# Kernel tuning notes

Hardware: AMD Instinct MI355X
Metric: run time of the kernel (lower is better)

Reference implementation:

```python
import jax, jax.numpy as jnp
import numpy as np

TEMPERATURE = 0.1
NEG_INF = -1e30  # finite sentinel so masked logsumexp has zero (not NaN) gradient


def setup_inputs() -> dict:
    key = jax.random.key(0)
    k1, k2, k3 = jax.random.split(key, 3)
    N, D = 8192, 512          # flattened (batch * TRs) trials, feature dim
    NUM_CLASSES = 3           # vigilance states
    return {
        "objs_feats": jax.random.normal(k1, (N, D), dtype=jnp.float32),
        "objs_labels": jax.random.randint(k2, (N,), 0, NUM_CLASSES, dtype=jnp.int32),
        "bad_tr": jax.random.randint(k3, (N,), 0, 2, dtype=jnp.int32),
    }


def reference(objs_feats, objs_labels, bad_tr):
    # Faithful vectorization of SetCriterion.contrastive_loss_batch_without_break.
    N = objs_feats.shape[0]
    f = objs_feats / jnp.linalg.norm(objs_feats, axis=-1, keepdims=True)
    S = (f @ f.T) / TEMPERATURE                      # [N, N] cosine-sim logits

    valid = bad_tr == 0                              # [N]
    same = objs_labels[:, None] == objs_labels[None, :]
    eye = jnp.eye(N, dtype=bool)
    neg_mask = valid[None, :] & (~same)              # [N, N] negatives per anchor
    pos_mask = valid[None, :] & same & (~eye)        # [N, N] positives per anchor

    has_neg = neg_mask.any(axis=1)
    has_pos = pos_mask.any(axis=1)
    processed = valid & has_neg                      # anchors the loop doesn't `continue` past

    # logsumexp over negatives of each anchor row
    neg_lse = jax.nn.logsumexp(jnp.where(neg_mask, S, NEG_INF), axis=1)  # [N]

    # anchors WITH positives: CE over rows [S[i,p], S[i, negs...]] with target 0,
    # averaged over positives p -> mean_p( logaddexp(S[i,p], neg_lse_i) - S[i,p] )
    ce_per_pos = jnp.logaddexp(S, neg_lse[:, None]) - S                  # [N, N]
    pos_cnt = pos_mask.sum(axis=1)
    loss_with_pos = jnp.where(pos_mask, ce_per_pos, 0.0).sum(axis=1) / jnp.maximum(pos_cnt, 1)

    # anchors WITHOUT positives: pos logit is the constant 1/temperature
    inv_t = jnp.float32(1.0 / TEMPERATURE)
    loss_no_pos = jnp.logaddexp(inv_t, neg_lse) - inv_t

    per_anchor = jnp.where(has_pos, loss_with_pos, loss_no_pos)
    total = jnp.where(processed, per_anchor, 0.0).sum()
    # valid_obj_cnt starts at 1; no-pos anchors net to 0 (−1 then +1)
    count = 1 + (processed & has_pos).sum()
    return total / count.astype(total.dtype)
```

## Files before the change

### kernel.cpp

```cpp
#include <hip/hip_runtime.h>

typedef __bf16 bf16x8 __attribute__((ext_vector_type(8)));
typedef __bf16 bf16x4 __attribute__((ext_vector_type(4)));
typedef float f32x4 __attribute__((ext_vector_type(4)));

#define SLOTW 260

#define GLOAD_LDS16(g, l)                                                      \
  __builtin_amdgcn_global_load_lds(                                            \
      (const __attribute__((address_space(1))) void*)(g),                      \
      (__attribute__((address_space(3))) void*)(l), 16, 0, 0)

__global__ __launch_bounds__(1024) void k_scan(
    const int* __restrict__ labels, const int* __restrict__ bad,
    unsigned char* __restrict__ code, int* __restrict__ dst,
    int* __restrict__ hdr, __bf16* __restrict__ fng,
    unsigned char* __restrict__ gcode, float* __restrict__ out, int Nv,
    int Dv) {
  const int t = threadIdx.x;
  const int lane = t & 63, wv = t >> 6;
  const int per = Nv >> 10;
  const int base = t * per;
  unsigned char lc[8];
  int cnt[3] = {0, 0, 0};
  for (int k = 0; k < per; ++k) {
    const int r = base + k;
    const unsigned char c =
        (bad[r] == 0) ? (unsigned char)labels[r] : (unsigned char)255;
    lc[k] = c;
    code[r] = c;
    if (c <= 2) cnt[c]++;
  }
  int inc0 = cnt[0], inc1 = cnt[1], inc2 = cnt[2];
#pragma unroll
  for (int off = 1; off < 64; off <<= 1) {
    const int a = __shfl_up(inc0, off);
    const int b = __shfl_up(inc1, off);
    const int c = __shfl_up(inc2, off);
    if (lane >= off) {
      inc0 += a;
      inc1 += b;
      inc2 += c;
    }
  }
  __shared__ int wt[16][3], wo[17][3];
  if (lane == 63) {
    wt[wv][0] = inc0;
    wt[wv][1] = inc1;
    wt[wv][2] = inc2;
  }
  __syncthreads();
  if (t == 0) {
    int s0 = 0, s1 = 0, s2 = 0;
    for (int w = 0; w < 16; ++w) {
      wo[w][0] = s0;
      wo[w][1] = s1;
      wo[w][2] = s2;
      s0 += wt[w][0];
      s1 += wt[w][1];
      s2 += wt[w][2];
    }
    wo[16][0] = s0;
    wo[16][1] = s1;
    wo[16][2] = s2;
  }
  __syncthreads();
  const int C0 = wo[16][0], C1 = wo[16][1], C2 = wo[16][2];
  int run[3];
  run[0] = wo[wv][0] + inc0 - cnt[0];
  run[1] = C0 + wo[wv][1] + inc1 - cnt[1];
  run[2] = C0 + C1 + wo[wv][2] + inc2 - cnt[2];
  for (int k = 0; k < per; ++k) {
    const int c = lc[k];
    dst[base + k] = (c <= 2) ? run[c]++ : -1;
  }
  const int M = C0 + C1 + C2;
  const int Mpad = (M + 127) & ~127;
  if (t == 0) {
    const int NTv = Mpad >> 7;
    hdr[0] = M;
    hdr[1] = Mpad;
    hdr[2] = NTv;
    hdr[3] = NTv * (NTv + 1) / 2;
    hdr[4] = C0;
    hdr[5] = C1;
    hdr[6] = C2;
    int count = 1;
    if (C0 >= 2 && M > C0) count += C0;
    if (C1 >= 2 && M > C1) count += C1;
    if (C2 >= 2 && M > C2) count += C2;
    hdr[7] = count;
    out[0] = 0.f;
  }
  for (int i = M + t; i < Mpad; i += 1024) gcode[i] = 255;
  const int nv4 = (Mpad - M) * (Dv >> 3);
  float4* fp = (float4*)(fng + (size_t)M * Dv);
  const float4 z = {0.f, 0.f, 0.f, 0.f};
  for (int i = t; i < nv4; i += 1024) fp[i] = z;
}

__global__ __launch_bounds__(128) void k_norm(const float* __restrict__ X,
                                              const unsigned char* __restrict__
                                                  code,
                                              const int* __restrict__ dst,
                                              __bf16* __restrict__ fng,
                                              unsigned char* __restrict__ gcode,
                                              int Dv) {
  const int row = blockIdx.x;
  const unsigned char c = code[row];
  if (c > 2) return;
  const int g = dst[row];
  const int t = threadIdx.x;
  const float4* xr = (const float4*)(X + (size_t)row * Dv);
  const int nv4 = Dv >> 2;
  __shared__ float sred[2];
  if (nv4 == 128) {
    const float4 v = xr[t];
    float ss = v.x * v.x + v.y * v.y + v.z * v.z + v.w * v.w;
#pragma unroll
    for (int off = 32; off; off >>= 1) ss += __shfl_down(ss, off);
    if ((t & 63) == 0) sred[t >> 6] = ss;
    __syncthreads();
    const float inv = 1.0f / sqrtf(sred[0] + sred[1]);
    bf16x4 o;
    o[0] = (__bf16)(v.x * inv);
    o[1] = (__bf16)(v.y * inv);
    o[2] = (__bf16)(v.z * inv);
    o[3] = (__bf16)(v.w * inv);
    *(bf16x4*)(fng + (size_t)g * Dv + t * 4) = o;
    if (t == 0) gcode[g] = c;
    return;
  }
  float ss = 0.f;
  for (int idx = t; idx < nv4; idx += 128) {
    float4 v = xr[idx];
    ss += v.x * v.x + v.y * v.y + v.z * v.z + v.w * v.w;
  }
#pragma unroll
  for (int off = 32; off; off >>= 1) ss += __shfl_down(ss, off);
  if ((t & 63) == 0) sred[t >> 6] = ss;
  __syncthreads();
  const float inv = 1.0f / sqrtf(sred[0] + sred[1]);
  const int nv8 = Dv >> 3;
  for (int idx = t; idx < nv8; idx += 128) {
    const float4 v0 = xr[idx * 2];
    const float4 v1 = xr[idx * 2 + 1];
    bf16x8 o;
    o[0] = (__bf16)(v0.x * inv);
    o[1] = (__bf16)(v0.y * inv);
    o[2] = (__bf16)(v0.z * inv);
    o[3] = (__bf16)(v0.w * inv);
    o[4] = (__bf16)(v1.x * inv);
    o[5] = (__bf16)(v1.y * inv);
    o[6] = (__bf16)(v1.z * inv);
    o[7] = (__bf16)(v1.w * inv);
    *(bf16x8*)(fng + (size_t)g * Dv + idx * 8) = o;
  }
  if (t == 0) gcode[g] = c;
}

__device__ __forceinline__ void tri_decode(int blk, int NT, int& bi, int& bj) {
  int b = 0, rem = blk, span = NT;
  while (rem >= span) {
    rem -= span;
    b++;
    span--;
  }
  bi = b;
  bj = b + rem;
}

__device__ __forceinline__ bool tile_overlap(const unsigned char* gcode,
                                             size_t sA, int lastA,
                                             size_t rowB) {
  const int la0 = gcode[sA], la1 = gcode[sA + lastA];
  const int lb0 = gcode[rowB], lb1 = gcode[rowB + 127];
  const int hiA = la1 > 2 ? 2 : la1;
  const int hiB = lb1 > 2 ? 2 : lb1;
  const int lo = la0 > lb0 ? la0 : lb0;
  const int hi = hiA < hiB ? hiA : hiB;
  return (la0 <= 2) && (lb0 <= 2) && (lo <= hi);
}

__global__ __launch_bounds__(512, 6) void k_p1(
    const __bf16* __restrict__ fng, const unsigned char* __restrict__ gcode,
    const int* __restrict__ hdr, float* __restrict__ P,
    _Float16* __restrict__ Sc, int Dv) {
  const int NTv = hdr[2];
  const int ntri = hdr[3];
  int bid = blockIdx.x;
  if (bid >= ntri) return;
  {
    const int q = ntri >> 3, r = ntri & 7, x = bid & 7, o = bid >> 3;
    bid = (x < r ? x * (q + 1) : r * (q + 1) + (x - r) * q) + o;
  }
  int bi, bj;
  tri_decode(bid, NTv, bi, bj);
  const size_t sA = (size_t)bi * 128;
  const size_t rowB = (size_t)bj * 128;
  __shared__ __align__(16) __bf16 As[2][128 * 32];
  __shared__ __align__(16) __bf16 Bs[2][128 * 32];

  const int t = threadIdx.x;
  const int lane = t & 63;
  const int wave = t >> 6;
  const int quad = lane >> 4;
  const int l16 = lane & 15;
  const int wr = (wave >> 1) * 32;
  const int wc = (wave & 1) * 64;
  const int r4 = t >> 2, q4 = t & 3;

  f32x4 acc[2][4] = {};
  auto stage = [&](int k0, int b) {
    GLOAD_LDS16(fng + (sA + r4) * Dv + k0 + q4 * 8,
                &As[b][(size_t)wave * 64 * 8]);
    GLOAD_LDS16(fng + (rowB + r4) * Dv + k0 + q4 * 8,
                &Bs[b][(size_t)wave * 64 * 8]);
  };
  stage(0, 0);
  int buf = 0;
  for (int k0 = 0; k0 < Dv; k0 += 32) {
    __syncthreads();
    if (k0 + 32 < Dv) stage(k0 + 32, buf ^ 1);
    bf16x8 af[2], bfv[4];
#pragma unroll
    for (int mi = 0; mi < 2; ++mi)
      af[mi] = *(const bf16x8*)&As[buf][(wr + mi * 16 + l16) * 32 + quad * 8];
#pragma unroll
    for (int ni = 0; ni < 4; ++ni)
      bfv[ni] = *(const bf16x8*)&Bs[buf][(wc + ni * 16 + l16) * 32 + quad * 8];
#pragma unroll
    for (int mi = 0; mi < 2; ++mi)
#pragma unroll
      for (int ni = 0; ni < 4; ++ni)
        acc[mi][ni] = __builtin_amdgcn_mfma_f32_16x16x32_bf16(
            af[mi], bfv[ni], acc[mi][ni], 0, 0, 0);
    buf ^= 1;
  }

  unsigned char ca[8], cb[4];
#pragma unroll
  for (int mi = 0; mi < 2; ++mi)
#pragma unroll
    for (int r = 0; r < 4; ++r)
      ca[mi * 4 + r] = gcode[sA + wr + mi * 16 + quad * 4 + r];
#pragma unroll
  for (int ni = 0; ni < 4; ++ni) cb[ni] = gcode[rowB + wc + ni * 16 + l16];
  const bool ov = tile_overlap(gcode, sA, 127, rowB);
  _Float16* St = Sc + (size_t)bid * 16384;

  float rowsum[8] = {};
  float colsum[4] = {};
#pragma unroll
  for (int mi = 0; mi < 2; ++mi)
#pragma unroll
    for (int ni = 0; ni < 4; ++ni)
#pragma unroll
      for (int r = 0; r < 4; ++r) {
        const float s = acc[mi][ni][r] * 10.0f;
        const float ex = __expf(s);
        const int a = ca[mi * 4 + r], b = cb[ni];
        const bool diff = a != b;
        rowsum[mi * 4 + r] += (b <= 2 && diff) ? ex : 0.f;
        colsum[ni] += (a <= 2 && diff) ? ex : 0.f;
        if (ov)
          St[(wr + mi * 16 + quad * 4 + r) * 128 + wc + ni * 16 + l16] =
              (_Float16)s;
      }
#pragma unroll
  for (int off = 1; off < 16; off <<= 1)
#pragma unroll
    for (int k = 0; k < 8; ++k) rowsum[k] += __shfl_xor(rowsum[k], off);
  if (l16 == 0)
#pragma unroll
    for (int k = 0; k < 8; ++k) {
      const size_t base =
          (sA + wr + (k >> 2) * 16 + quad * 4 + (k & 3)) * SLOTW + bj * 4;
      P[base + (wave & 1)] = rowsum[k];
      P[base + 2 + (wave & 1)] = 0.f;
    }
  if (bi != bj) {
#pragma unroll
    for (int off = 16; off < 64; off <<= 1)
#pragma unroll
      for (int ni = 0; ni < 4; ++ni) colsum[ni] += __shfl_xor(colsum[ni], off);
    if (quad == 0)
#pragma unroll
      for (int ni = 0; ni < 4; ++ni)
        P[(rowB + wc + ni * 16 + l16) * SLOTW + bi * 4 + (wave >> 1)] =
            colsum[ni];
  }
}

__global__ __launch_bounds__(256) void k_red(const float* __restrict__ P,
                                             float* __restrict__ out,
                                             const int* __restrict__ hdr,
                                             int Nv) {
  const int g = blockIdx.x * 256 + threadIdx.x;
  if (g >= Nv || g >= hdr[1]) return;
  const int ns = hdr[2] * 4;
  float s = 0.f;
  const float4* p = (const float4*)(P + (size_t)g * SLOTW);
  for (int k = 0; k < (ns >> 2); ++k) {
    const float4 v = p[k];
    s += v.x + v.y + v.z + v.w;
  }
  out[g] = s;
}

__global__ __launch_bounds__(256) void k_p2(
    const unsigned char* __restrict__ gcode, const int* __restrict__ hdr,
    const float* __restrict__ E, float* __restrict__ P2,
    const _Float16* __restrict__ Sc) {
  const int NTv = hdr[2];
  if ((int)blockIdx.x >= hdr[3]) return;
  int bi, bj;
  tri_decode(blockIdx.x, NTv, bi, bj);
  const int h = blockIdx.y;
  const size_t sA = (size_t)bi * 128 + h * 64;
  const size_t rowB = (size_t)bj * 128;
  const int t = threadIdx.x;
  const bool diag = (bi == bj);

  if (!tile_overlap(gcode, sA, 63, rowB)) {
    if (t < 64) {
      const size_t base = (sA + t) * SLOTW + bj * 4;
      P2[base] = 0.f;
      P2[base + 1] = 0.f;
      P2[base + 2] = 0.f;
      P2[base + 3] = 0.f;
    } else if (t < 192 && !diag) {
      const size_t base = (rowB + t - 64) * SLOTW + bi * 4 + h * 2;
      P2[base] = 0.f;
      P2[base + 1] = 0.f;
    }
    return;
  }

  const _Float16* St = Sc + ((size_t)blockIdx.x * 2 + h) * 8192;
  const int l8 = t & 15;
  unsigned char cb[8];
  float eB[8];
  {
    const uint2 cv = *(const uint2*)(gcode + rowB + l8 * 8);
    const unsigned char* cp = (const unsigned char*)&cv;
#pragma unroll
    for (int e = 0; e < 8; ++e) cb[e] = cp[e];
    const float4 e0 = *(const float4*)(E + rowB + l8 * 8);
    const float4 e1 = *(const float4*)(E + rowB + l8 * 8 + 4);
    eB[0] = e0.x; eB[1] = e0.y; eB[2] = e0.z; eB[3] = e0.w;
    eB[4] = e1.x; eB[5] = e1.y; eB[6] = e1.z; eB[7] = e1.w;
  }
  float colsum[8] = {};
#pragma unroll
  for (int k = 0; k < 4; ++k) {
    const int row = k * 16 + (t >> 4);
    const int a = gcode[sA + row];
    const float eA = E[sA + row];
    const float4 sv = *(const float4*)(St + row * 128 + l8 * 8);
    const _Float16* hp = (const _Float16*)&sv;
    float rsum = 0.f;
#pragma unroll
    for (int e = 0; e < 8; ++e) {
      const int col = l8 * 8 + e;
      const float em = __expf(-(float)hp[e]);
      const bool pos =
          (a == cb[e]) && (cb[e] <= 2) && !(diag && (row + h * 64) == col);
      rsum += pos ? __logf(1.f + eA * em) : 0.f;
      colsum[e] += pos ? __logf(1.f + eB[e] * em) : 0.f;
    }
#pragma unroll
    for (int off = 1; off < 16; off <<= 1) rsum += __shfl_xor(rsum, off);
    if (l8 == 0) {
      const size_t base = (sA + row) * SLOTW + bj * 4;
      P2[base + h * 2] = rsum;
      P2[base + h * 2 + 1] = 0.f;
      P2[base + (1 - h) * 2] = 0.f;
      P2[base + (1 - h) * 2 + 1] = 0.f;
    }
  }
  __shared__ float colpart[128 * 17];
#pragma unroll
  for (int e = 0; e < 8; ++e) colpart[(l8 * 8 + e) * 17 + (t >> 4)] = colsum[e];
  __syncthreads();
  if (t < 128 && !diag) {
    float cs = 0.f;
#pragma unroll
    for (int i = 0; i < 16; ++i) cs += colpart[t * 17 + i];
    const size_t base = (rowB + t) * SLOTW + bi * 4 + h * 2;
    P2[base] = cs;
    P2[base + 1] = 0.f;
  }
}

__global__ __launch_bounds__(256) void k_fin(const float* __restrict__ P2,
                                             const float* __restrict__ E,
                                             const unsigned char* __restrict__
                                                 gcode,
                                             const int* __restrict__ hdr,
                                             float* __restrict__ out) {
  const int g = blockIdx.x * 256 + threadIdx.x;
  const int t = threadIdx.x;
  float contrib = 0.f;
  if (g < hdr[1]) {
    const int l = gcode[g];
    if (l <= 2) {
      const int c0 = hdr[4], c1 = hdr[5], c2 = hdr[6];
      const int vt = c0 + c1 + c2;
      const int cmy = (l == 0) ? c0 : ((l == 1) ? c1 : c2);
      if (vt - cmy > 0) {
        const int pos_cnt = cmy - 1;
        if (pos_cnt > 0) {
          const int ns = hdr[2] * 4;
          float s = 0.f;
          const float4* p = (const float4*)(P2 + (size_t)g * SLOTW);
          for (int k = 0; k < (ns >> 2); ++k) {
            const float4 v = p[k];
            s += v.x + v.y + v.z + v.w;
          }
          contrib = s / (float)pos_cnt;
        } else {
          contrib = __logf(1.f + E[g] * __expf(-10.0f));
        }
      }
    }
  }
#pragma unroll
  for (int off = 32; off; off >>= 1) contrib += __shfl_down(contrib, off);
  __shared__ float sd[4];
  if ((t & 63) == 0) sd[t >> 6] = contrib;
  __syncthreads();
  if (t == 0) {
    const float tot = sd[0] + sd[1] + sd[2] + sd[3];
    atomicAdd(out, tot / (float)hdr[7]);
  }
}

extern "C" void kernel_launch(void* const* d_in, const int* in_sizes, int n_in,
                              void* d_out, int out_size, void* d_ws,
                              size_t ws_size, hipStream_t stream) {
  const float* X = (const float*)d_in[0];
  const int* labels = (const int*)d_in[1];
  const int* bad = (const int*)d_in[2];
  const int Nv = in_sizes[1];
  const int Dv = in_sizes[0] / Nv;

  size_t off = 0;
  auto alloc = [&](size_t bytes) -> void* {
    size_t p = (off + 255) & ~(size_t)255;
    off = p + bytes;
    return (void*)((char*)d_ws + p);
  };
  const int NT = Nv / 128;
  const int ntri_max = NT * (NT + 1) / 2;
  __bf16* fng = (__bf16*)alloc((size_t)Nv * Dv * 2);
  float* P = (float*)alloc((size_t)Nv * SLOTW * 4);
  float* P2 = (float*)alloc((size_t)Nv * SLOTW * 4);
  _Float16* Sc = (_Float16*)alloc((size_t)ntri_max * 2 * 8192 * 2);
  float* E = (float*)alloc((size_t)Nv * 4);
  int* dst = (int*)alloc((size_t)Nv * 4);
  unsigned char* code = (unsigned char*)alloc((size_t)Nv);
  unsigned char* gcode = (unsigned char*)alloc((size_t)Nv);
  int* hdr = (int*)alloc(64);
  if (off > ws_size) return;

  k_scan<<<1, 1024, 0, stream>>>(labels, bad, code, dst, hdr, fng, gcode,
                                 (float*)d_out, Nv, Dv);
  k_norm<<<Nv, 128, 0, stream>>>(X, code, dst, fng, gcode, Dv);
  k_p1<<<ntri_max, 512, 0, stream>>>(fng, gcode, hdr, P, Sc, Dv);
  k_red<<<(Nv + 255) / 256, 256, 0, stream>>>(P, E, hdr, Nv);
  dim3 gp(ntri_max, 2);
  k_p2<<<gp, 256, 0, stream>>>(gcode, hdr, E, P2, Sc);
  k_fin<<<(Nv + 255) / 256, 256, 0, stream>>>(P2, E, gcode, hdr,
                                              (float*)d_out);
}
```

Baseline: 140.5 us.

## Fuse all stages into one persistent cooperative kernel with grid syncs

Replaces the six-kernel pipeline (scan, normalize, GEMM+exp sums, reduce, positive-pair pass, finalize) with a single cooperative persistent kernel that uses grid.sync between phases. The goal is to remove launch gaps and tail effects between kernels. The fused kernel folds the E reduction into the second pass per tile and processes full 128x128 tiles instead of half tiles. It falls back to the old launches if the cooperative launch fails. Grid-wide barriers and grid-stride loops over a fixed occupancy-sized grid may cost load balance, and the LDS sizing may cap occupancy.

```diff
diff --git a/kernel.cpp b/kernel.cpp
--- a/kernel.cpp
+++ b/kernel.cpp
@@ -1,4 +1,7 @@
 #include <hip/hip_runtime.h>
+#include <hip/hip_cooperative_groups.h>
+
+namespace cg = cooperative_groups;
 
 typedef __bf16 bf16x8 __attribute__((ext_vector_type(8)));
 typedef __bf16 bf16x4 __attribute__((ext_vector_type(4)));
@@ -10,6 +13,419 @@
   __builtin_amdgcn_global_load_lds(                                            \
       (const __attribute__((address_space(1))) void*)(g),                      \
       (__attribute__((address_space(3))) void*)(l), 16, 0, 0)
+
+__device__ __forceinline__ void tri_decode(int blk, int NT, int& bi, int& bj) {
+  int b = 0, rem = blk, span = NT;
+  while (rem >= span) {
+    rem -= span;
+    b++;
+    span--;
+  }
+  bi = b;
+  bj = b + rem;
+}
+
+__device__ __forceinline__ int xcd_swz(int w, int n) {
+  const int q = n >> 3, r = n & 7, x = w & 7, o = w >> 3;
+  return (x < r ? x * (q + 1) : r * (q + 1) + (x - r) * q) + o;
+}
+
+__device__ __forceinline__ bool tile_overlap(const unsigned char* gcode,
+                                             size_t sA, int lastA,
+                                             size_t rowB) {
+  const int la0 = gcode[sA], la1 = gcode[sA + lastA];
+  const int lb0 = gcode[rowB], lb1 = gcode[rowB + 127];
+  const int hiA = la1 > 2 ? 2 : la1;
+  const int hiB = lb1 > 2 ? 2 : lb1;
+  const int lo = la0 > lb0 ? la0 : lb0;
+  const int hi = hiA < hiB ? hiA : hiB;
+  return (la0 <= 2) && (lb0 <= 2) && (lo <= hi);
+}
+
+__global__ __launch_bounds__(512, 6) void k_fused(
+    const float* __restrict__ X, const int* __restrict__ labels,
+    const int* __restrict__ bad, unsigned char* __restrict__ code,
+    int* __restrict__ dst, int* __restrict__ hdr, __bf16* __restrict__ fng,
+    unsigned char* __restrict__ gcode, float* __restrict__ P,
+    _Float16* __restrict__ Sc, float* __restrict__ P2,
+    float* __restrict__ out, int Nv, int Dv) {
+  const int t = threadIdx.x;
+  const int G = gridDim.x;
+  cg::grid_group grid = cg::this_grid();
+
+  __shared__ __align__(16) char smem[33792];
+  auto As = (__bf16(*)[128 * 32])smem;
+  auto Bs = (__bf16(*)[128 * 32])(smem + 16384);
+  float* colpart = (float*)smem;
+  float* E_s = (float*)(smem + 32768);
+  __shared__ int wt[8][3], wo[9][3];
+  __shared__ float sd[8];
+
+  if (blockIdx.x == 0) {
+    const int lane = t & 63, wv = t >> 6;
+    const int per = Nv >> 9;
+    const int base = t * per;
+    unsigned char lc[16];
+    int cnt[3] = {0, 0, 0};
+    for (int k = 0; k < per; ++k) {
+      const int r = base + k;
+      const unsigned char c =
+          (bad[r] == 0) ? (unsigned char)labels[r] : (unsigned char)255;
+      lc[k] = c;
+      code[r] = c;
+      if (c <= 2) cnt[c]++;
+    }
+    int inc0 = cnt[0], inc1 = cnt[1], inc2 = cnt[2];
+#pragma unroll
+    for (int off = 1; off < 64; off <<= 1) {
+      const int a = __shfl_up(inc0, off);
+      const int b = __shfl_up(inc1, off);
+      const int c = __shfl_up(inc2, off);
+      if (lane >= off) {
+        inc0 += a;
+        inc1 += b;
+        inc2 += c;
+      }
+    }
+    if (lane == 63) {
+      wt[wv][0] = inc0;
+      wt[wv][1] = inc1;
+      wt[wv][2] = inc2;
+    }
+    __syncthreads();
+    if (t == 0) {
+      int s0 = 0, s1 = 0, s2 = 0;
+      for (int w = 0; w < 8; ++w) {
+        wo[w][0] = s0;
+        wo[w][1] = s1;
+        wo[w][2] = s2;
+        s0 += wt[w][0];
+        s1 += wt[w][1];
+        s2 += wt[w][2];
+      }
+      wo[8][0] = s0;
+      wo[8][1] = s1;
+      wo[8][2] = s2;
+    }
+    __syncthreads();
+    const int C0 = wo[8][0], C1 = wo[8][1], C2 = wo[8][2];
+    int run[3];
+    run[0] = wo[wv][0] + inc0 - cnt[0];
+    run[1] = C0 + wo[wv][1] + inc1 - cnt[1];
+    run[2] = C0 + C1 + wo[wv][2] + inc2 - cnt[2];
+    for (int k = 0; k < per; ++k) {
+      const int c = lc[k];
+      dst[base + k] = (c <= 2) ? run[c]++ : -1;
+    }
+    const int Ml = C0 + C1 + C2;
+    const int Mpadl = (Ml + 127) & ~127;
+    if (t == 0) {
+      const int NTl = Mpadl >> 7;
+      hdr[0] = Ml;
+      hdr[1] = Mpadl;
+      hdr[2] = NTl;
+      hdr[3] = NTl * (NTl + 1) / 2;
+      hdr[4] = C0;
+      hdr[5] = C1;
+      hdr[6] = C2;
+      int count = 1;
+      if (C0 >= 2 && Ml > C0) count += C0;
+      if (C1 >= 2 && Ml > C1) count += C1;
+      if (C2 >= 2 && Ml > C2) count += C2;
+      hdr[7] = count;
+      out[0] = 0.f;
+    }
+    for (int i = Ml + t; i < Mpadl; i += 512) gcode[i] = 255;
+  }
+  grid.sync();
+
+  const int M = hdr[0], Mpad = hdr[1], NTv = hdr[2], ntri = hdr[3];
+
+  {
+    const int rsub = t >> 6, tl = t & 63;
+    const int nw = Nv >> 3;
+    if (Dv == 512) {
+      for (int w = blockIdx.x; w < nw; w += G) {
+        const int row = w * 8 + rsub;
+        const unsigned char c = code[row];
+        float4 v0 = {0.f, 0.f, 0.f, 0.f}, v1 = {0.f, 0.f, 0.f, 0.f};
+        float ss = 0.f;
+        if (c <= 2) {
+          const float4* xr = (const float4*)(X + (size_t)row * Dv);
+          v0 = xr[tl * 2];
+          v1 = xr[tl * 2 + 1];
+          ss = v0.x * v0.x + v0.y * v0.y + v0.z * v0.z + v0.w * v0.w +
+               v1.x * v1.x + v1.y * v1.y + v1.z * v1.z + v1.w * v1.w;
+        }
+#pragma unroll
+        for (int off = 32; off; off >>= 1) ss += __shfl_down(ss, off);
+        ss = __shfl(ss, 0);
+        if (c <= 2) {
+          const float inv = 1.0f / sqrtf(ss);
+          const int g = dst[row];
+          bf16x8 o;
+          o[0] = (__bf16)(v0.x * inv);
+          o[1] = (__bf16)(v0.y * inv);
+          o[2] = (__bf16)(v0.z * inv);
+          o[3] = (__bf16)(v0.w * inv);
+          o[4] = (__bf16)(v1.x * inv);
+          o[5] = (__bf16)(v1.y * inv);
+          o[6] = (__bf16)(v1.z * inv);
+          o[7] = (__bf16)(v1.w * inv);
+          *(bf16x8*)(fng + (size_t)g * Dv + tl * 8) = o;
+          if (tl == 0) gcode[g] = c;
+        }
+      }
+    } else {
+      for (int w = blockIdx.x; w < nw; w += G) {
+        const int row = w * 8 + rsub;
+        const unsigned char c = code[row];
+        if (c <= 2) {
+          const float4* xr = (const float4*)(X + (size_t)row * Dv);
+          float ss = 0.f;
+          for (int idx = tl; idx < (Dv >> 2); idx += 64) {
+            const float4 v = xr[idx];
+            ss += v.x * v.x + v.y * v.y + v.z * v.z + v.w * v.w;
+          }
+#pragma unroll
+          for (int off = 32; off; off >>= 1) ss += __shfl_down(ss, off);
+          ss = __shfl(ss, 0);
+          const float inv = 1.0f / sqrtf(ss);
+          const int g = dst[row];
+          for (int idx = tl; idx < (Dv >> 3); idx += 64) {
+            const float4 u0 = xr[idx * 2];
+            const float4 u1 = xr[idx * 2 + 1];
+            bf16x8 o;
+            o[0] = (__bf16)(u0.x * inv);
+            o[1] = (__bf16)(u0.y * inv);
+            o[2] = (__bf16)(u0.z * inv);
+            o[3] = (__bf16)(u0.w * inv);
+            o[4] = (__bf16)(u1.x * inv);
+            o[5] = (__bf16)(u1.y * inv);
+            o[6] = (__bf16)(u1.z * inv);
+            o[7] = (__bf16)(u1.w * inv);
+            *(bf16x8*)(fng + (size_t)g * Dv + idx * 8) = o;
+          }
+          if (tl == 0) gcode[g] = c;
+        }
+      }
+    }
+    const int npad = (Mpad - M) * (Dv >> 3);
+    float4* fp = (float4*)(fng + (size_t)M * Dv);
+    const float4 z = {0.f, 0.f, 0.f, 0.f};
+    for (int i = blockIdx.x * 512 + t; i < npad; i += G * 512) fp[i] = z;
+  }
+  grid.sync();
+
+  {
+    const int lane = t & 63;
+    const int wave = t >> 6;
+    const int quad = lane >> 4;
+    const int l16 = lane & 15;
+    const int wr = (wave >> 1) * 32;
+    const int wc = (wave & 1) * 64;
+    const int r4 = t >> 2, q4 = t & 3;
+    for (int w = blockIdx.x; w < ntri; w += G) {
+      const int bid = xcd_swz(w, ntri);
+      int bi, bj;
+      tri_decode(bid, NTv, bi, bj);
+      const size_t sA = (size_t)bi * 128;
+      const size_t rowB = (size_t)bj * 128;
+      f32x4 acc[2][4] = {};
+      auto stage = [&](int k0, int b) {
+        GLOAD_LDS16(fng + (sA + r4) * Dv + k0 + q4 * 8,
+                    &As[b][(size_t)wave * 64 * 8]);
+        GLOAD_LDS16(fng + (rowB + r4) * Dv + k0 + q4 * 8,
+                    &Bs[b][(size_t)wave * 64 * 8]);
+      };
+      stage(0, 0);
+      int buf = 0;
+      for (int k0 = 0; k0 < Dv; k0 += 32) {
+        __syncthreads();
+        if (k0 + 32 < Dv) stage(k0 + 32, buf ^ 1);
+        bf16x8 af[2], bfv[4];
+#pragma unroll
+        for (int mi = 0; mi < 2; ++mi)
+          af[mi] =
+              *(const bf16x8*)&As[buf][(wr + mi * 16 + l16) * 32 + quad * 8];
+#pragma unroll
+        for (int ni = 0; ni < 4; ++ni)
+          bfv[ni] =
+              *(const bf16x8*)&Bs[buf][(wc + ni * 16 + l16) * 32 + quad * 8];
+#pragma unroll
+        for (int mi = 0; mi < 2; ++mi)
+#pragma unroll
+          for (int ni = 0; ni < 4; ++ni)
+            acc[mi][ni] = __builtin_amdgcn_mfma_f32_16x16x32_bf16(
+                af[mi], bfv[ni], acc[mi][ni], 0, 0, 0);
+        buf ^= 1;
+      }
+      unsigned char ca[8], cb[4];
+#pragma unroll
+      for (int mi = 0; mi < 2; ++mi)
+#pragma unroll
+        for (int r = 0; r < 4; ++r)
+          ca[mi * 4 + r] = gcode[sA + wr + mi * 16 + quad * 4 + r];
+#pragma unroll
+      for (int ni = 0; ni < 4; ++ni) cb[ni] = gcode[rowB + wc + ni * 16 + l16];
+      const bool ov = tile_overlap(gcode, sA, 127, rowB);
+      _Float16* St = Sc + (size_t)bid * 16384;
+
+      float rowsum[8] = {};
+      float colsum[4] = {};
+#pragma unroll
+      for (int mi = 0; mi < 2; ++mi)
+#pragma unroll
+        for (int ni = 0; ni < 4; ++ni)
+#pragma unroll
+          for (int r = 0; r < 4; ++r) {
+            const float s = acc[mi][ni][r] * 10.0f;
+            const float ex = __expf(s);
+            const int a = ca[mi * 4 + r], b = cb[ni];
+            const bool diff = a != b;
+            rowsum[mi * 4 + r] += (b <= 2 && diff) ? ex : 0.f;
+            colsum[ni] += (a <= 2 && diff) ? ex : 0.f;
+            if (ov)
+              St[(wr + mi * 16 + quad * 4 + r) * 128 + wc + ni * 16 + l16] =
+                  (_Float16)s;
+          }
+#pragma unroll
+      for (int off = 1; off < 16; off <<= 1)
+#pragma unroll
+        for (int k = 0; k < 8; ++k) rowsum[k] += __shfl_xor(rowsum[k], off);
+      if (l16 == 0)
+#pragma unroll
+        for (int k = 0; k < 8; ++k) {
+          const size_t base =
+              (sA + wr + (k >> 2) * 16 + quad * 4 + (k & 3)) * SLOTW + bj * 4;
+          P[base + (wave & 1)] = rowsum[k];
+          P[base + 2 + (wave & 1)] = 0.f;
+        }
+      if (bi != bj) {
+#pragma unroll
+        for (int off = 16; off < 64; off <<= 1)
+#pragma unroll
+          for (int ni = 0; ni < 4; ++ni)
+            colsum[ni] += __shfl_xor(colsum[ni], off);
+        if (quad == 0)
+#pragma unroll
+          for (int ni = 0; ni < 4; ++ni)
+            P[(rowB + wc + ni * 16 + l16) * SLOTW + bi * 4 + (wave >> 1)] =
+                colsum[ni];
+      }
+    }
+  }
+  grid.sync();
+
+  {
+    const int l8 = t & 15;
+    const int rq = t >> 4;
+    for (int w = blockIdx.x; w < ntri; w += G) {
+      const int bid = xcd_swz(w, ntri);
+      int bi, bj;
+      tri_decode(bid, NTv, bi, bj);
+      const size_t sA = (size_t)bi * 128;
+      const size_t rowB = (size_t)bj * 128;
+      const bool diag = (bi == bj);
+      if (!tile_overlap(gcode, sA, 127, rowB)) {
+        if (t < 128)
+          P2[(sA + t) * SLOTW + bj] = 0.f;
+        else if (t < 256 && !diag)
+          P2[(rowB + t - 128) * SLOTW + bi] = 0.f;
+        continue;
+      }
+      {
+        const int rr = t >> 1, half = t & 1;
+        const size_t g = (rr < 128) ? (sA + rr) : (rowB + (rr - 128));
+        const float2* p = (const float2*)(P + g * SLOTW + half * 2 * NTv);
+        float s = 0.f;
+        for (int k = 0; k < NTv; ++k) s += p[k].x + p[k].y;
+        s += __shfl_xor(s, 1);
+        if (half == 0) E_s[rr] = s;
+      }
+      __syncthreads();
+      const _Float16* St = Sc + (size_t)bid * 16384;
+      unsigned char cbv[8];
+      float eB[8];
+      {
+        const uint2 cv = *(const uint2*)(gcode + rowB + l8 * 8);
+        const unsigned char* cp = (const unsigned char*)&cv;
+#pragma unroll
+        for (int e = 0; e < 8; ++e) cbv[e] = cp[e];
+#pragma unroll
+        for (int e = 0; e < 8; ++e) eB[e] = E_s[128 + l8 * 8 + e];
+      }
+      float colsum[8] = {};
+#pragma unroll
+      for (int k = 0; k < 4; ++k) {
+        const int row = k * 32 + rq;
+        const int a = gcode[sA + row];
+        const float eA = E_s[row];
+        const float4 sv = *(const float4*)(St + (size_t)row * 128 + l8 * 8);
+        const _Float16* hp = (const _Float16*)&sv;
+        float rsum = 0.f;
+#pragma unroll
+        for (int e = 0; e < 8; ++e) {
+          const int col = l8 * 8 + e;
+          const float em = __expf(-(float)hp[e]);
+          const bool pos =
+              (a == cbv[e]) && (cbv[e] <= 2) && !(diag && row == col);
+          rsum += pos ? __logf(1.f + eA * em) : 0.f;
+          colsum[e] += pos ? __logf(1.f + eB[e] * em) : 0.f;
+        }
+#pragma unroll
+        for (int off = 1; off < 16; off <<= 1) rsum += __shfl_xor(rsum, off);
+        if (l8 == 0) P2[(sA + row) * SLOTW + bj] = rsum;
+      }
+#pragma unroll
+      for (int e = 0; e < 8; ++e) colpart[rq * 132 + l8 * 8 + e] = colsum[e];
+      __syncthreads();
+      if (t < 128 && !diag) {
+        float cs = 0.f;
+#pragma unroll
+        for (int i = 0; i < 32; ++i) cs += colpart[i * 132 + t];
+        P2[(rowB + t) * SLOTW + bi] = cs;
+      }
+    }
+  }
+  grid.sync();
+
+  {
+    const int c0 = hdr[4], c1 = hdr[5], c2 = hdr[6], cntv = hdr[7];
+    const int vt = c0 + c1 + c2;
+    float contrib = 0.f;
+    for (int g = blockIdx.x * 512 + t; g < M; g += G * 512) {
+      const int l = gcode[g];
+      if (l <= 2) {
+        const int cmy = (l == 0) ? c0 : ((l == 1) ? c1 : c2);
+        if (vt - cmy > 0) {
+          const int pos_cnt = cmy - 1;
+          if (pos_cnt > 0) {
+            float s = 0.f;
+            const float* p = P2 + (size_t)g * SLOTW;
+            for (int k = 0; k < NTv; ++k) s += p[k];
+            contrib += s / (float)pos_cnt;
+          } else {
+            float e2 = 0.f;
+            const float2* p = (const float2*)(P + (size_t)g * SLOTW);
+            for (int k = 0; k < 2 * NTv; ++k) e2 += p[k].x + p[k].y;
+            contrib += __logf(1.f + e2 * __expf(-10.0f));
+          }
+        }
+      }
+    }
+#pragma unroll
+    for (int off = 32; off; off >>= 1) contrib += __shfl_down(contrib, off);
+    if ((t & 63) == 0) sd[t >> 6] = contrib;
+    __syncthreads();
+    if (t == 0) {
+      float tot = 0.f;
+#pragma unroll
+      for (int i = 0; i < 8; ++i) tot += sd[i];
+      if (tot != 0.f) atomicAdd(out, tot / (float)cntv);
+    }
+  }
+}
 
 __global__ __launch_bounds__(1024) void k_scan(
     const int* __restrict__ labels, const int* __restrict__ bad,
@@ -159,29 +575,6 @@
   if (t == 0) gcode[g] = c;
 }
 
-__device__ __forceinline__ void tri_decode(int blk, int NT, int& bi, int& bj) {
-  int b = 0, rem = blk, span = NT;
-  while (rem >= span) {
-    rem -= span;
-    b++;
-    span--;
-  }
-  bi = b;
-  bj = b + rem;
-}
-
-__device__ __forceinline__ bool tile_overlap(const unsigned char* gcode,
-                                             size_t sA, int lastA,
-                                             size_t rowB) {
-  const int la0 = gcode[sA], la1 = gcode[sA + lastA];
-  const int lb0 = gcode[rowB], lb1 = gcode[rowB + 127];
-  const int hiA = la1 > 2 ? 2 : la1;
-  const int hiB = lb1 > 2 ? 2 : lb1;
-  const int lo = la0 > lb0 ? la0 : lb0;
-  const int hi = hiA < hiB ? hiA : hiB;
-  return (la0 <= 2) && (lb0 <= 2) && (lo <= hi);
-}
-
 __global__ __launch_bounds__(512, 6) void k_p1(
     const __bf16* __restrict__ fng, const unsigned char* __restrict__ gcode,
     const int* __restrict__ hdr, float* __restrict__ P,
@@ -190,10 +583,7 @@
   const int ntri = hdr[3];
   int bid = blockIdx.x;
   if (bid >= ntri) return;
-  {
-    const int q = ntri >> 3, r = ntri & 7, x = bid & 7, o = bid >> 3;
-    bid = (x < r ? x * (q + 1) : r * (q + 1) + (x - r) * q) + o;
-  }
+  bid = xcd_swz(bid, ntri);
   int bi, bj;
   tri_decode(bid, NTv, bi, bj);
   const size_t sA = (size_t)bi * 128;
@@ -237,7 +627,6 @@
             af[mi], bfv[ni], acc[mi][ni], 0, 0, 0);
     buf ^= 1;
   }
-
   unsigned char ca[8], cb[4];
 #pragma unroll
   for (int mi = 0; mi < 2; ++mi)
@@ -313,9 +702,11 @@
     const float* __restrict__ E, float* __restrict__ P2,
     const _Float16* __restrict__ Sc) {
   const int NTv = hdr[2];
-  if ((int)blockIdx.x >= hdr[3]) return;
+  const int ntri = hdr[3];
+  if ((int)blockIdx.x >= ntri) return;
+  const int bid = xcd_swz(blockIdx.x, ntri);
   int bi, bj;
-  tri_decode(blockIdx.x, NTv, bi, bj);
+  tri_decode(bid, NTv, bi, bj);
   const int h = blockIdx.y;
   const size_t sA = (size_t)bi * 128 + h * 64;
   const size_t rowB = (size_t)bj * 128;
@@ -337,7 +728,7 @@
     return;
   }
 
-  const _Float16* St = Sc + ((size_t)blockIdx.x * 2 + h) * 8192;
+  const _Float16* St = Sc + ((size_t)bid * 2 + h) * 8192;
   const int l8 = t & 15;
   unsigned char cb[8];
   float eB[8];
@@ -463,14 +854,35 @@
   unsigned char* gcode = (unsigned char*)alloc((size_t)Nv);
   int* hdr = (int*)alloc(64);
   if (off > ws_size) return;
+  float* outp = (float*)d_out;
+
+  static int occ = -1;
+  if (occ < 0) {
+    int o = 0;
+    if (hipOccupancyMaxActiveBlocksPerMultiprocessor(&o, k_fused, 512, 0) !=
+        hipSuccess)
+      o = 0;
+    occ = o;
+  }
+  if (occ >= 1) {
+    int G = occ * 256;
+    int NvA = Nv, DvA = Dv;
+    void* args[] = {(void*)&X,    (void*)&labels, (void*)&bad,  (void*)&code,
+                    (void*)&dst,  (void*)&hdr,    (void*)&fng,  (void*)&gcode,
+                    (void*)&P,    (void*)&Sc,     (void*)&P2,   (void*)&outp,
+                    (void*)&NvA,  (void*)&DvA};
+    if (hipLaunchCooperativeKernel(k_fused, dim3(G), dim3(512), args, 0,
+                                   stream) == hipSuccess)
+      return;
+    (void)hipGetLastError();
+  }
 
   k_scan<<<1, 1024, 0, stream>>>(labels, bad, code, dst, hdr, fng, gcode,
-                                 (float*)d_out, Nv, Dv);
+                                 outp, Nv, Dv);
   k_norm<<<Nv, 128, 0, stream>>>(X, code, dst, fng, gcode, Dv);
   k_p1<<<ntri_max, 512, 0, stream>>>(fng, gcode, hdr, P, Sc, Dv);
   k_red<<<(Nv + 255) / 256, 256, 0, stream>>>(P, E, hdr, Nv);
   dim3 gp(ntri_max, 2);
   k_p2<<<gp, 256, 0, stream>>>(gcode, hdr, E, P2, Sc);
-  k_fin<<<(Nv + 255) / 256, 256, 0, stream>>>(P2, E, gcode, hdr,
-                                              (float*)d_out);
-}
+  k_fin<<<(Nv + 255) / 256, 256, 0, stream>>>(P2, E, gcode, hdr, outp);
+}
```

New measurement: 312.0 us. +122.1%, slower.

## Transpose partial-sum buffers to slot-major layout and use wave-per-row normalization

Applied to the files above, without the earlier changes.

The per-row partial sum buffers P and P2 change from row-major with padded slot width to slot-major [slot][Nv]. Reductions in k_red and k_fin then read coalesced across threads, and k_p1 writes row sums as float4 vectors. k_norm now handles one row per wavefront, eight rows per block, so it needs no shared-memory reduction or barrier. The risk is that column-sum and P2 writes become scattered single floats with stride Nv.

```diff
diff --git a/kernel.cpp b/kernel.cpp
--- a/kernel.cpp
+++ b/kernel.cpp
@@ -3,13 +3,12 @@
 typedef __bf16 bf16x8 __attribute__((ext_vector_type(8)));
 typedef __bf16 bf16x4 __attribute__((ext_vector_type(4)));
 typedef float f32x4 __attribute__((ext_vector_type(4)));
-
-#define SLOTW 260
 
 #define GLOAD_LDS16(g, l)                                                      \
   __builtin_amdgcn_global_load_lds(                                            \
       (const __attribute__((address_space(1))) void*)(g),                      \
       (__attribute__((address_space(3))) void*)(l), 16, 0, 0)
+
 
 __global__ __launch_bounds__(1024) void k_scan(
     const int* __restrict__ labels, const int* __restrict__ bad,
@@ -99,52 +98,29 @@
   for (int i = t; i < nv4; i += 1024) fp[i] = z;
 }
 
-__global__ __launch_bounds__(128) void k_norm(const float* __restrict__ X,
+__global__ __launch_bounds__(512) void k_norm(const float* __restrict__ X,
                                               const unsigned char* __restrict__
                                                   code,
                                               const int* __restrict__ dst,
                                               __bf16* __restrict__ fng,
                                               unsigned char* __restrict__ gcode,
-                                              int Dv) {
-  const int row = blockIdx.x;
+                                              int Nv, int Dv) {
+  const int t = threadIdx.x;
+  const int tl = t & 63;
+  const int row = blockIdx.x * 8 + (t >> 6);
+  if (row >= Nv) return;
   const unsigned char c = code[row];
   if (c > 2) return;
-  const int g = dst[row];
-  const int t = threadIdx.x;
   const float4* xr = (const float4*)(X + (size_t)row * Dv);
-  const int nv4 = Dv >> 2;
-  __shared__ float sred[2];
-  if (nv4 == 128) {
-    const float4 v = xr[t];
-    float ss = v.x * v.x + v.y * v.y + v.z * v.z + v.w * v.w;
-#pragma unroll
-    for (int off = 32; off; off >>= 1) ss += __shfl_down(ss, off);
-    if ((t & 63) == 0) sred[t >> 6] = ss;
-    __syncthreads();
-    const float inv = 1.0f / sqrtf(sred[0] + sred[1]);
-    bf16x4 o;
-    o[0] = (__bf16)(v.x * inv);
-    o[1] = (__bf16)(v.y * inv);
-    o[2] = (__bf16)(v.z * inv);
-    o[3] = (__bf16)(v.w * inv);
-    *(bf16x4*)(fng + (size_t)g * Dv + t * 4) = o;
-    if (t == 0) gcode[g] = c;
-    return;
-  }
-  float ss = 0.f;
-  for (int idx = t; idx < nv4; idx += 128) {
-    float4 v = xr[idx];
-    ss += v.x * v.x + v.y * v.y + v.z * v.z + v.w * v.w;
-  }
-#pragma unroll
-  for (int off = 32; off; off >>= 1) ss += __shfl_down(ss, off);
-  if ((t & 63) == 0) sred[t >> 6] = ss;
-  __syncthreads();
-  const float inv = 1.0f / sqrtf(sred[0] + sred[1]);
-  const int nv8 = Dv >> 3;
-  for (int idx = t; idx < nv8; idx += 128) {
-    const float4 v0 = xr[idx * 2];
-    const float4 v1 = xr[idx * 2 + 1];
+  if (Dv == 512) {
+    const float4 v0 = xr[tl * 2];
+    const float4 v1 = xr[tl * 2 + 1];
+    float ss = v0.x * v0.x + v0.y * v0.y + v0.z * v0.z + v0.w * v0.w +
+               v1.x * v1.x + v1.y * v1.y + v1.z * v1.z + v1.w * v1.w;
+#pragma unroll
+    for (int off = 1; off < 64; off <<= 1) ss += __shfl_xor(ss, off);
+    const float inv = 1.0f / sqrtf(ss);
+    const int g = dst[row];
     bf16x8 o;
     o[0] = (__bf16)(v0.x * inv);
     o[1] = (__bf16)(v0.y * inv);
@@ -154,9 +130,34 @@
     o[5] = (__bf16)(v1.y * inv);
     o[6] = (__bf16)(v1.z * inv);
     o[7] = (__bf16)(v1.w * inv);
+    *(bf16x8*)(fng + (size_t)g * Dv + tl * 8) = o;
+    if (tl == 0) gcode[g] = c;
+    return;
+  }
+  float ss = 0.f;
+  for (int idx = tl; idx < (Dv >> 2); idx += 64) {
+    const float4 v = xr[idx];
+    ss += v.x * v.x + v.y * v.y + v.z * v.z + v.w * v.w;
+  }
+#pragma unroll
+  for (int off = 1; off < 64; off <<= 1) ss += __shfl_xor(ss, off);
+  const float inv = 1.0f / sqrtf(ss);
+  const int g = dst[row];
+  for (int idx = tl; idx < (Dv >> 3); idx += 64) {
+    const float4 u0 = xr[idx * 2];
+    const float4 u1 = xr[idx * 2 + 1];
+    bf16x8 o;
+    o[0] = (__bf16)(u0.x * inv);
+    o[1] = (__bf16)(u0.y * inv);
+    o[2] = (__bf16)(u0.z * inv);
+    o[3] = (__bf16)(u0.w * inv);
+    o[4] = (__bf16)(u1.x * inv);
+    o[5] = (__bf16)(u1.y * inv);
+    o[6] = (__bf16)(u1.z * inv);
+    o[7] = (__bf16)(u1.w * inv);
     *(bf16x8*)(fng + (size_t)g * Dv + idx * 8) = o;
   }
-  if (t == 0) gcode[g] = c;
+  if (tl == 0) gcode[g] = c;
 }
 
 __device__ __forceinline__ void tri_decode(int blk, int NT, int& bi, int& bj) {
@@ -168,6 +169,11 @@
   }
   bi = b;
   bj = b + rem;
+}
+
+__device__ __forceinline__ int xcd_swz(int w, int n) {
+  const int q = n >> 3, r = n & 7, x = w & 7, o = w >> 3;
+  return (x < r ? x * (q + 1) : r * (q + 1) + (x - r) * q) + o;
 }
 
 __device__ __forceinline__ bool tile_overlap(const unsigned char* gcode,
@@ -185,15 +191,12 @@
 __global__ __launch_bounds__(512, 6) void k_p1(
     const __bf16* __restrict__ fng, const unsigned char* __restrict__ gcode,
     const int* __restrict__ hdr, float* __restrict__ P,
-    _Float16* __restrict__ Sc, int Dv) {
+    _Float16* __restrict__ Sc, int Nv, int Dv) {
   const int NTv = hdr[2];
   const int ntri = hdr[3];
   int bid = blockIdx.x;
   if (bid >= ntri) return;
-  {
-    const int q = ntri >> 3, r = ntri & 7, x = bid & 7, o = bid >> 3;
-    bid = (x < r ? x * (q + 1) : r * (q + 1) + (x - r) * q) + o;
-  }
+  bid = xcd_swz(bid, ntri);
   int bi, bj;
   tri_decode(bid, NTv, bi, bj);
   const size_t sA = (size_t)bi * 128;
@@ -237,7 +240,6 @@
             af[mi], bfv[ni], acc[mi][ni], 0, 0, 0);
     buf ^= 1;
   }
-
   unsigned char ca[8], cb[4];
 #pragma unroll
   for (int mi = 0; mi < 2; ++mi)
@@ -271,24 +273,29 @@
   for (int off = 1; off < 16; off <<= 1)
 #pragma unroll
     for (int k = 0; k < 8; ++k) rowsum[k] += __shfl_xor(rowsum[k], off);
-  if (l16 == 0)
-#pragma unroll
-    for (int k = 0; k < 8; ++k) {
-      const size_t base =
-          (sA + wr + (k >> 2) * 16 + quad * 4 + (k & 3)) * SLOTW + bj * 4;
-      P[base + (wave & 1)] = rowsum[k];
-      P[base + 2 + (wave & 1)] = 0.f;
-    }
+  if (l16 == 0) {
+    const int sreal = bj * 4 + (wave & 1);
+    const int szero = bj * 4 + 2 + (wave & 1);
+    const size_t r0 = sA + wr + quad * 4;
+    float4 v0 = {rowsum[0], rowsum[1], rowsum[2], rowsum[3]};
+    float4 v1 = {rowsum[4], rowsum[5], rowsum[6], rowsum[7]};
+    const float4 z = {0.f, 0.f, 0.f, 0.f};
+    *(float4*)(P + (size_t)sreal * Nv + r0) = v0;
+    *(float4*)(P + (size_t)sreal * Nv + r0 + 16) = v1;
+    *(float4*)(P + (size_t)szero * Nv + r0) = z;
+    *(float4*)(P + (size_t)szero * Nv + r0 + 16) = z;
+  }
   if (bi != bj) {
 #pragma unroll
     for (int off = 16; off < 64; off <<= 1)
 #pragma unroll
       for (int ni = 0; ni < 4; ++ni) colsum[ni] += __shfl_xor(colsum[ni], off);
-    if (quad == 0)
+    if (quad == 0) {
+      const int s = bi * 4 + (wave >> 1);
 #pragma unroll
       for (int ni = 0; ni < 4; ++ni)
-        P[(rowB + wc + ni * 16 + l16) * SLOTW + bi * 4 + (wave >> 1)] =
-            colsum[ni];
+        P[(size_t)s * Nv + rowB + wc + ni * 16 + l16] = colsum[ni];
+    }
   }
 }
 
@@ -299,19 +306,22 @@
   const int g = blockIdx.x * 256 + threadIdx.x;
   if (g >= Nv || g >= hdr[1]) return;
   const int ns = hdr[2] * 4;
-  float s = 0.f;
-  const float4* p = (const float4*)(P + (size_t)g * SLOTW);
-  for (int k = 0; k < (ns >> 2); ++k) {
-    const float4 v = p[k];
-    s += v.x + v.y + v.z + v.w;
-  }
-  out[g] = s;
+  float s0 = 0.f, s1 = 0.f, s2 = 0.f, s3 = 0.f;
+  int k = 0;
+  for (; k + 4 <= ns; k += 4) {
+    s0 += P[(size_t)k * Nv + g];
+    s1 += P[(size_t)(k + 1) * Nv + g];
+    s2 += P[(size_t)(k + 2) * Nv + g];
+    s3 += P[(size_t)(k + 3) * Nv + g];
+  }
+  for (; k < ns; ++k) s0 += P[(size_t)k * Nv + g];
+  out[g] = (s0 + s1) + (s2 + s3);
 }
 
 __global__ __launch_bounds__(256) void k_p2(
     const unsigned char* __restrict__ gcode, const int* __restrict__ hdr,
     const float* __restrict__ E, float* __restrict__ P2,
-    const _Float16* __restrict__ Sc) {
+    const _Float16* __restrict__ Sc, int Nv) {
   const int NTv = hdr[2];
   if ((int)blockIdx.x >= hdr[3]) return;
   int bi, bj;
@@ -324,15 +334,15 @@
 
   if (!tile_overlap(gcode, sA, 63, rowB)) {
     if (t < 64) {
-      const size_t base = (sA + t) * SLOTW + bj * 4;
-      P2[base] = 0.f;
-      P2[base + 1] = 0.f;
-      P2[base + 2] = 0.f;
-      P2[base + 3] = 0.f;
+      const size_t r = sA + t;
+      P2[(size_t)(bj * 4 + 0) * Nv + r] = 0.f;
+      P2[(size_t)(bj * 4 + 1) * Nv + r] = 0.f;
+      P2[(size_t)(bj * 4 + 2) * Nv + r] = 0.f;
+      P2[(size_t)(bj * 4 + 3) * Nv + r] = 0.f;
     } else if (t < 192 && !diag) {
-      const size_t base = (rowB + t - 64) * SLOTW + bi * 4 + h * 2;
-      P2[base] = 0.f;
-      P2[base + 1] = 0.f;
+      const size_t r = rowB + t - 64;
+      P2[(size_t)(bi * 4 + h * 2) * Nv + r] = 0.f;
+      P2[(size_t)(bi * 4 + h * 2 + 1) * Nv + r] = 0.f;
     }
     return;
   }
@@ -372,11 +382,11 @@
 #pragma unroll
     for (int off = 1; off < 16; off <<= 1) rsum += __shfl_xor(rsum, off);
     if (l8 == 0) {
-      const size_t base = (sA + row) * SLOTW + bj * 4;
-      P2[base + h * 2] = rsum;
-      P2[base + h * 2 + 1] = 0.f;
-      P2[base + (1 - h) * 2] = 0.f;
-      P2[base + (1 - h) * 2 + 1] = 0.f;
+      const size_t r = sA + row;
+      P2[(size_t)(bj * 4 + h * 2) * Nv + r] = rsum;
+      P2[(size_t)(bj * 4 + h * 2 + 1) * Nv + r] = 0.f;
+      P2[(size_t)(bj * 4 + (1 - h) * 2) * Nv + r] = 0.f;
+      P2[(size_t)(bj * 4 + (1 - h) * 2 + 1) * Nv + r] = 0.f;
     }
   }
   __shared__ float colpart[128 * 17];
@@ -387,9 +397,9 @@
     float cs = 0.f;
 #pragma unroll
     for (int i = 0; i < 16; ++i) cs += colpart[t * 17 + i];
-    const size_t base = (rowB + t) * SLOTW + bi * 4 + h * 2;
-    P2[base] = cs;
-    P2[base + 1] = 0.f;
+    const size_t r = rowB + t;
+    P2[(size_t)(bi * 4 + h * 2) * Nv + r] = cs;
+    P2[(size_t)(bi * 4 + h * 2 + 1) * Nv + r] = 0.f;
   }
 }
 
@@ -398,7 +408,7 @@
                                              const unsigned char* __restrict__
                                                  gcode,
                                              const int* __restrict__ hdr,
-                                             float* __restrict__ out) {
+                                             float* __restrict__ out, int Nv) {
   const int g = blockIdx.x * 256 + threadIdx.x;
   const int t = threadIdx.x;
   float contrib = 0.f;
@@ -412,13 +422,16 @@
         const int pos_cnt = cmy - 1;
         if (pos_cnt > 0) {
           const int ns = hdr[2] * 4;
-          float s = 0.f;
-          const float4* p = (const float4*)(P2 + (size_t)g * SLOTW);
-          for (int k = 0; k < (ns >> 2); ++k) {
-            const float4 v = p[k];
-            s += v.x + v.y + v.z + v.w;
+          float s0 = 0.f, s1 = 0.f, s2 = 0.f, s3 = 0.f;
+          int k = 0;
+          for (; k + 4 <= ns; k += 4) {
+            s0 += P2[(size_t)k * Nv + g];
+            s1 += P2[(size_t)(k + 1) * Nv + g];
+            s2 += P2[(size_t)(k + 2) * Nv + g];
+            s3 += P2[(size_t)(k + 3) * Nv + g];
           }
-          contrib = s / (float)pos_cnt;
+          for (; k < ns; ++k) s0 += P2[(size_t)k * Nv + g];
+          contrib = ((s0 + s1) + (s2 + s3)) / (float)pos_cnt;
         } else {
           contrib = __logf(1.f + E[g] * __expf(-10.0f));
         }
@@ -454,8 +467,8 @@
   const int NT = Nv / 128;
   const int ntri_max = NT * (NT + 1) / 2;
   __bf16* fng = (__bf16*)alloc((size_t)Nv * Dv * 2);
-  float* P = (float*)alloc((size_t)Nv * SLOTW * 4);
-  float* P2 = (float*)alloc((size_t)Nv * SLOTW * 4);
+  float* P = (float*)alloc((size_t)Nv * 256 * 4);
+  float* P2 = (float*)alloc((size_t)Nv * 256 * 4);
   _Float16* Sc = (_Float16*)alloc((size_t)ntri_max * 2 * 8192 * 2);
   float* E = (float*)alloc((size_t)Nv * 4);
   int* dst = (int*)alloc((size_t)Nv * 4);
@@ -463,14 +476,14 @@
   unsigned char* gcode = (unsigned char*)alloc((size_t)Nv);
   int* hdr = (int*)alloc(64);
   if (off > ws_size) return;
+  float* outp = (float*)d_out;
 
   k_scan<<<1, 1024, 0, stream>>>(labels, bad, code, dst, hdr, fng, gcode,
-                                 (float*)d_out, Nv, Dv);
-  k_norm<<<Nv, 128, 0, stream>>>(X, code, dst, fng, gcode, Dv);
-  k_p1<<<ntri_max, 512, 0, stream>>>(fng, gcode, hdr, P, Sc, Dv);
+                                 outp, Nv, Dv);
+  k_norm<<<(Nv + 7) / 8, 512, 0, stream>>>(X, code, dst, fng, gcode, Nv, Dv);
+  k_p1<<<ntri_max, 512, 0, stream>>>(fng, gcode, hdr, P, Sc, Nv, Dv);
   k_red<<<(Nv + 255) / 256, 256, 0, stream>>>(P, E, hdr, Nv);
   dim3 gp(ntri_max, 2);
-  k_p2<<<gp, 256, 0, stream>>>(gcode, hdr, E, P2, Sc);
-  k_fin<<<(Nv + 255) / 256, 256, 0, stream>>>(P2, E, gcode, hdr,
-                                              (float*)d_out);
-}
+  k_p2<<<gp, 256, 0, stream>>>(gcode, hdr, E, P2, Sc, Nv);
+  k_fin<<<(Nv + 255) / 256, 256, 0, stream>>>(P2, E, gcode, hdr, outp, Nv);
+}
```

New measurement: 135.1 us. 3.8% less time.
